# Optimization experiments

Measured on AMD Instinct MI355X. Metric: run time of the kernel, lower is better.

Reference implementation:

```python
import jax, jax.numpy as jnp
import numpy as np

B, P, C = 32, 8732, 21
TOP_K = 200
CONF_THRESH = 0.01
NMS_THRESH = 0.45
VAR0, VAR1 = 0.1, 0.2  # VOC PRIOR_BOX VARIANCE


def setup_inputs() -> dict:
    key = jax.random.key(0)
    k1, k2, k3 = jax.random.split(key, 3)
    loc_data = jax.random.normal(k1, (B, P, 4), jnp.float32)
    conf_data = jax.random.uniform(k2, (B, P, C), jnp.float32)
    prior_data = jax.random.uniform(k3, (P, 4), jnp.float32)
    return {"loc_data": loc_data, "conf_data": conf_data, "prior_data": prior_data}


def _decode(loc, priors):
    # priors are (cx, cy, w, h); returns (x1, y1, x2, y2)
    cxcy = priors[:, :2] + loc[:, :2] * VAR0 * priors[:, 2:]
    wh = priors[:, 2:] * jnp.exp(loc[:, 2:] * VAR1)
    x1y1 = cxcy - wh * 0.5
    return jnp.concatenate([x1y1, x1y1 + wh], axis=1)  # [P,4]


def _nms_class(boxes, scores):
    # boxes [P,4], scores [P] -> [TOP_K,5] rows of (score, x1, y1, x2, y2)
    s = jnp.where(scores > CONF_THRESH, scores, -1.0)
    top_s, idx = jax.lax.top_k(s, TOP_K)          # descending scores
    b = boxes[idx]                                 # [K,4]
    valid = top_s > CONF_THRESH
    x1, y1, x2, y2 = b[:, 0], b[:, 1], b[:, 2], b[:, 3]
    area = (x2 - x1) * (y2 - y1)
    # pairwise intersection / IoU [K,K]
    xx1 = jnp.maximum(x1[:, None], x1[None, :])
    yy1 = jnp.maximum(y1[:, None], y1[None, :])
    xx2 = jnp.minimum(x2[:, None], x2[None, :])
    yy2 = jnp.minimum(y2[:, None], y2[None, :])
    inter = jnp.clip(xx2 - xx1, 0.0) * jnp.clip(yy2 - yy1, 0.0)
    union = area[:, None] + area[None, :] - inter
    iou = inter / union
    ar = jnp.arange(TOP_K)

    def step(carry, j):
        kept, suppressed = carry
        is_kept = valid[j] & ~suppressed[j]
        kept = kept.at[j].set(is_kept)
        suppressed = suppressed | (is_kept & (iou[j] > NMS_THRESH) & (ar > j))
        return (kept, suppressed), None

    (kept, _), _ = jax.lax.scan(
        step, (jnp.zeros(TOP_K, bool), jnp.zeros(TOP_K, bool)), ar)
    # compact kept rows to the front (matches output[i, cl, :count] = ...)
    pos = jnp.cumsum(kept) - 1
    safe = jnp.where(kept, pos, TOP_K)
    rows = jnp.concatenate([top_s[:, None], b], axis=1)  # [K,5]
    out = jnp.zeros((TOP_K + 1, 5), rows.dtype).at[safe].set(rows)[:TOP_K]
    return out


def reference(loc_data, conf_data, prior_data):
    def per_image(loc, conf):
        boxes = _decode(loc, prior_data)           # [P,4]
        return jax.vmap(lambda s: _nms_class(boxes, s), in_axes=1)(conf)  # [C,K,5]

    out = jax.vmap(per_image)(loc_data, conf_data)  # [B,C,K,5]
    return out.at[:, 0].set(0.0)  # class 0 (background) is skipped in original
```

## Files before the change

kernel.cpp:

```cpp
#include <hip/hip_runtime.h>
#include <stdint.h>

#define B_ 32
#define P_ 8732
#define C_ 21
#define TOPK 200
#define TGT 228
#define TGT0 300
#define SUBCAP 28
#define NCH2 35
#define NSLOT (NCH2 * SUBCAP)
#define CONF_T 0.01f
#define NMS_T 0.45f
#define NT 512
#define KV4 5
#define NTASK (B_ * C_)

__device__ __forceinline__ uint32_t f2s(float f) {
    uint32_t u = __float_as_uint(f);
    return (u & 0x80000000u) ? ~u : (u | 0x80000000u);
}
__device__ __forceinline__ float s2f(uint32_t s) {
    uint32_t b = (s & 0x80000000u) ? (s & 0x7FFFFFFFu) : ~s;
    return __uint_as_float(b);
}
__device__ __forceinline__ uint32_t keyof(float v) {
    return f2s((v > CONF_T) ? v : -1.0f);
}
__device__ __forceinline__ uint32_t thr0() {
    return f2s(1.0f - (float)TGT0 / (float)P_);
}

__global__ __launch_bounds__(256) void scatter_cands(const float* __restrict__ conf,
                                                     uint32_t* __restrict__ gccnt,
                                                     uint64_t* __restrict__ gcand) {
    const int b = blockIdx.x / NCH2;
    const int ch = blockIdx.x % NCH2;
    const int p0 = ch * 256;
    const int n = min(256, P_ - p0);
    const int tid = threadIdx.x;
    const int lane = tid & 63;
    const int cs = tid >> 6;
    __shared__ float tile[256 * C_];
    const float4* src4 = (const float4*)(conf + ((size_t)b * P_ + p0) * C_);
    float4* tile4 = (float4*)tile;
    const int tot4 = (n * C_) >> 2;
    for (int i = tid; i < tot4; i += 256) tile4[i] = src4[i];
    __syncthreads();
    const uint32_t T0 = thr0();
    const bool act = (4 * lane) < n;
    for (int c = (cs == 0 ? 4 : cs); c < C_; c += 4) {
        uint32_t kk[4];
        int nq = 0;
        if (act) {
            const float* tp = &tile[4 * lane * C_ + c];
            kk[0] = keyof(tp[0 * C_]);
            kk[1] = keyof(tp[1 * C_]);
            kk[2] = keyof(tp[2 * C_]);
            kk[3] = keyof(tp[3 * C_]);
            nq = (kk[0] >= T0) + (kk[1] >= T0) + (kk[2] >= T0) + (kk[3] >= T0);
        }
        int incl = nq;
        #pragma unroll
        for (int d = 1; d < 64; d <<= 1) {
            int v = __shfl_up(incl, d);
            if (lane >= d) incl += v;
        }
        const int excl = incl - nq;
        const int total = __shfl(incl, 63);
        const int task = b * C_ + c;
        uint64_t* dst = gcand + ((size_t)task * NCH2 + ch) * SUBCAP;
        if (nq) {
            int pos = excl;
            const int pb = p0 + 4 * lane;
            #pragma unroll
            for (int k = 0; k < 4; ++k) {
                if (kk[k] >= T0) {
                    if (pos < SUBCAP)
                        dst[pos] = ((uint64_t)kk[k] << 32) | (uint32_t)(~(uint32_t)(pb + k));
                    ++pos;
                }
            }
        }
        if (lane == 0) gccnt[(size_t)task * NCH2 + ch] = (uint32_t)total;
    }
}

template<bool HASWS>
__global__ __launch_bounds__(NT, 6) void detect_kernel(
    const float* __restrict__ loc, const float* __restrict__ prior,
    const uint32_t* __restrict__ gccnt, const uint64_t* __restrict__ gcand,
    const float* __restrict__ conf, float* __restrict__ out)
{
    const int task = blockIdx.x;
    const int b = task / C_;
    const int c = task % C_;
    const int tid = threadIdx.x;
    const int lane = tid & 63;
    float* outp = out + (size_t)task * TOPK * 5;

    if (c == 0) {
        for (int e = tid; e < TOPK * 5; e += NT) outp[e] = 0.0f;
        return;
    }

    __shared__ uint64_t cand[256];
    __shared__ float4 bbox[TOPK];
    __shared__ float bs[TOPK];
    __shared__ unsigned long long msk[TOPK * 4];
    __shared__ unsigned long long vmask[4];
    __shared__ int order[TOPK];
    __shared__ int s_cnt, s_nk;
    __shared__ int s_c2[2];
    __shared__ uint32_t s_ccnt[NCH2];
    __shared__ int s_gc, s_bad;

    const uint32_t T0 = thr0();

    if (tid == 0) s_cnt = 0;
    if (tid < 2) s_c2[tid] = 0;
    if (HASWS && tid < NCH2) s_ccnt[tid] = gccnt[(size_t)task * NCH2 + tid];
    for (int i2 = tid; i2 < TOPK * 4; i2 += NT) msk[i2] = 0ull;
    __syncthreads();
    if (HASWS && tid < 64) {
        uint32_t cc = (lane < NCH2) ? s_ccnt[lane] : 0u;
        int bad = (cc > SUBCAP) ? 1 : 0;
        int tot = (int)cc;
        #pragma unroll
        for (int d = 1; d < 64; d <<= 1) {
            tot += __shfl_down(tot, d);
            bad |= __shfl_down(bad, d);
        }
        if (lane == 0) { s_gc = tot; s_bad = bad; }
    }
    __syncthreads();

    const bool fast = HASWS && !s_bad && s_gc >= TOPK;
    const int gc = HASWS ? s_gc : 0;

    uint64_t vc0 = 0, vc1 = 0;
    bool val0 = false, val1 = false;
    uint4 kv[KV4];
    if (fast) {
        const uint64_t* gp = gcand + (size_t)task * NSLOT;
        {
            const int ch0 = tid / SUBCAP, i0 = tid - ch0 * SUBCAP;
            if (i0 < (int)s_ccnt[ch0]) { vc0 = gp[tid]; val0 = true; }
        }
        const int s1 = tid + NT;
        if (s1 < NSLOT) {
            const int ch1 = s1 / SUBCAP, i1 = s1 - ch1 * SUBCAP;
            if (i1 < (int)s_ccnt[ch1]) { vc1 = gp[s1]; val1 = true; }
        }
    } else {
        const float* sp = conf + (size_t)b * P_ * C_ + c;
        #pragma unroll
        for (int r = 0; r < KV4; ++r) {
            uint32_t uu[4];
            #pragma unroll
            for (int c4 = 0; c4 < 4; ++c4) {
                int p = (tid + r * NT) * 4 + c4;
                if (p < P_) {
                    float v = sp[(size_t)p * C_];
                    v = (v > CONF_T) ? v : -1.0f;
                    uu[c4] = f2s(v);
                } else uu[c4] = 0u;
            }
            kv[r] = make_uint4(uu[0], uu[1], uu[2], uu[3]);
        }
    }

    if (fast) {
        uint32_t vthr = T0;
        if (gc > 256) {
            const uint32_t k0 = (uint32_t)(vc0 >> 32);
            const uint32_t k1 = (uint32_t)(vc1 >> 32);
            uint32_t lo = T0, hi = 0xFFFFFFFFu;
            uint32_t t;
            {
                const float sc = s2f(T0);
                const float sn = 1.0f - (1.0f - sc) * (float)TGT / (float)gc;
                t = f2s(sn);
                if (!(t > lo && t < hi)) t = lo + ((hi - lo) >> 1);
            }
            for (int it = 0; ; ++it) {
                const int slot = it & 1;
                int my = (val0 && k0 >= t) + (val1 && k1 >= t);
                #pragma unroll
                for (int d = 1; d < 64; d <<= 1) my += __shfl_down(my, d);
                if (lane == 0) atomicAdd(&s_c2[slot], my);
                __syncthreads();
                const int cnt = s_c2[slot];
                __syncthreads();
                if (tid == 0) s_c2[slot] = 0;
                if (cnt >= TOPK && cnt <= 256) { vthr = t; break; }
                if (cnt > 256) lo = t; else hi = t;
                if (hi - lo <= 1) { vthr = lo; break; }
                uint32_t tn = 0;
                bool bis = (it >= 8) || (cnt == 0);
                if (!bis) {
                    const float sc = s2f(t);
                    const float sn = 1.0f - (1.0f - sc) * (float)TGT / (float)cnt;
                    tn = f2s(sn);
                    if (!(tn > lo && tn < hi)) bis = true;
                }
                if (bis) tn = lo + ((hi - lo) >> 1);
                t = tn;
            }
        }
        if (val0 && (uint32_t)(vc0 >> 32) >= vthr) {
            int pos = atomicAdd(&s_cnt, 1);
            if (pos < 256) cand[pos] = vc0;
        }
        if (val1 && (uint32_t)(vc1 >> 32) >= vthr) {
            int pos = atomicAdd(&s_cnt, 1);
            if (pos < 256) cand[pos] = vc1;
        }
    } else {
        uint32_t lo = 0u, hi = 0xFFFFFFFFu;
        uint32_t t = f2s(1.0f - (float)TGT / (float)P_);
        uint32_t vthr = 0u;
        for (int it = 0; ; ++it) {
            const int slot = it & 1;
            int my = 0;
            #pragma unroll
            for (int r = 0; r < KV4; ++r)
                my += (kv[r].x >= t) + (kv[r].y >= t) + (kv[r].z >= t) + (kv[r].w >= t);
            #pragma unroll
            for (int d = 1; d < 64; d <<= 1) my += __shfl_down(my, d);
            if (lane == 0) atomicAdd(&s_c2[slot], my);
            __syncthreads();
            const int cnt = s_c2[slot];
            __syncthreads();
            if (tid == 0) s_c2[slot] = 0;
            if (cnt >= TOPK && cnt <= 256) { vthr = t; break; }
            if (cnt > 256) lo = t; else hi = t;
            if (hi - lo <= 1) { vthr = lo; break; }
            uint32_t tn = 0;
            bool bis = (it >= 8) || (cnt == 0);
            if (!bis) {
                const float sc = s2f(t);
                const float sn = 1.0f - (1.0f - sc) * (float)TGT / (float)cnt;
                tn = f2s(sn);
                if (!(tn > lo && tn < hi)) bis = true;
            }
            if (bis) tn = lo + ((hi - lo) >> 1);
            t = tn;
        }
        #pragma unroll
        for (int r = 0; r < KV4; ++r) {
            const int pb = (tid + r * NT) * 4;
            uint32_t uu[4] = {kv[r].x, kv[r].y, kv[r].z, kv[r].w};
            #pragma unroll
            for (int c4 = 0; c4 < 4; ++c4) {
                uint32_t u = uu[c4];
                if (u >= vthr) {
                    int pos = atomicAdd(&s_cnt, 1);
                    if (pos < 256) cand[pos] = ((uint64_t)u << 32) | (uint32_t)(~(uint32_t)(pb + c4));
                }
            }
        }
    }
    __syncthreads();
    if (tid < 256 && tid >= s_cnt) cand[tid] = 0ull;
    __syncthreads();

    uint64_t v = (tid < 256) ? cand[tid] : 0ull;
    for (int kk = 2; kk <= 256; kk <<= 1) {
        for (int j = kk >> 1; j > 0; j >>= 1) {
            if (j >= 64) {
                __syncthreads();
                if (tid < 256) cand[tid] = v;
                __syncthreads();
                if (tid < 256) {
                    uint64_t pv = cand[tid ^ j];
                    bool keepmax = (((tid & j) == 0) == ((tid & kk) == 0));
                    v = keepmax ? (v > pv ? v : pv) : (v < pv ? v : pv);
                }
            } else if (tid < 256) {
                uint64_t pv = __shfl_xor(v, j);
                bool keepmax = (((tid & j) == 0) == ((tid & kk) == 0));
                v = keepmax ? (v > pv ? v : pv) : (v < pv ? v : pv);
            }
        }
    }

    float my_sc = -1.0f;
    if (tid < TOPK) {
        uint32_t su = (uint32_t)(v >> 32);
        int p = (int)(~(uint32_t)v);
        my_sc = s2f(su);
        const float4 l4 = *(const float4*)(loc + ((size_t)b * P_ + p) * 4);
        const float4 pr = *(const float4*)(prior + (size_t)p * 4);
        float cx = __fadd_rn(pr.x, __fmul_rn(__fmul_rn(l4.x, 0.1f), pr.z));
        float cy = __fadd_rn(pr.y, __fmul_rn(__fmul_rn(l4.y, 0.1f), pr.w));
        float ew = (float)exp((double)__fmul_rn(l4.z, 0.2f));
        float eh = (float)exp((double)__fmul_rn(l4.w, 0.2f));
        float w  = __fmul_rn(pr.z, ew);
        float h  = __fmul_rn(pr.w, eh);
        float x1 = __fsub_rn(cx, __fmul_rn(w, 0.5f));
        float y1 = __fsub_rn(cy, __fmul_rn(h, 0.5f));
        float x2 = __fadd_rn(x1, w);
        float y2 = __fadd_rn(y1, h);
        bs[tid] = my_sc;
        bbox[tid] = make_float4(x1, y1, x2, y2);
    }
    {
        unsigned long long bm = __ballot(tid < TOPK && my_sc > CONF_T);
        if (lane == 0 && tid < 256) vmask[tid >> 6] = bm;
    }
    __syncthreads();

    if (tid < 500) {
        const int rp = tid / 5;
        const int s  = tid - rp * 5;
        #pragma unroll
        for (int pass = 0; pass < 2; ++pass) {
            const int j  = pass ? (199 - rp) : rp;
            const int i0 = j + 1 + s;
            const float4 bj = bbox[j];
            const float  aj = __fmul_rn(__fsub_rn(bj.z, bj.x), __fsub_rn(bj.w, bj.y));
            for (int i = i0; i < TOPK; i += 5) {
                const float4 bi = bbox[i];
                float xx1 = fmaxf(bj.x, bi.x);
                float yy1 = fmaxf(bj.y, bi.y);
                float xx2 = fminf(bj.z, bi.z);
                float yy2 = fminf(bj.w, bi.w);
                float dx = fmaxf(__fsub_rn(xx2, xx1), 0.0f);
                float dy = fmaxf(__fsub_rn(yy2, yy1), 0.0f);
                float inter = __fmul_rn(dx, dy);
                if (inter > 0.0f) {
                    float ai = __fmul_rn(__fsub_rn(bi.z, bi.x), __fsub_rn(bi.w, bi.y));
                    float uni = __fsub_rn(__fadd_rn(aj, ai), inter);
                    float t45 = __fmul_rn(NMS_T, uni);
                    float mar = __fmul_rn(t45, 1e-6f);
                    bool sup;
                    if (inter > __fadd_rn(t45, mar)) sup = true;
                    else if (inter < __fsub_rn(t45, mar)) sup = false;
                    else sup = (inter / uni > NMS_T);
                    if (sup) atomicOr(&msk[j * 4 + (i >> 6)], 1ull << (i & 63));
                }
            }
        }
    }
    __syncthreads();

    if (tid < 64) {
        const int L = tid;
        auto or_reduce = [&](unsigned long long x) {
            #pragma unroll
            for (int d = 1; d < 64; d <<= 1) x |= __shfl_xor(x, d);
            return x;
        };
        unsigned long long s1 = 0, s2 = 0, s3 = 0;
        int nk = 0;
        #pragma unroll
        for (int w = 0; w < 4; ++w) {
            const int j = (w << 6) | L;
            unsigned long long r0 = 0, r1 = 0, r2 = 0, r3 = 0;
            if (j < TOPK) {
                const unsigned long long* mr = &msk[j * 4];
                r0 = mr[0]; r1 = mr[1]; r2 = mr[2]; r3 = mr[3];
            }
            const unsigned long long rself = (w == 0) ? r0 : (w == 1) ? r1
                                           : (w == 2) ? r2 : r3;
            unsigned long long sw = (w == 0) ? 0ull : (w == 1) ? s1
                                  : (w == 2) ? s2 : s3;
            unsigned long long alive = vmask[w] & ~sw;
            unsigned long long pm = 0;
            while (alive) {
                int jl = __ffsll(alive) - 1;
                if (L == 0) order[nk] = (w << 6) | jl;
                ++nk;
                sw |= __shfl(rself, jl);
                pm |= (1ull << jl);
                alive &= ~(sw | (1ull << jl));
            }
            if (pm) {
                const bool picked = (pm >> L) & 1ull;
                if (w == 0) {
                    s1 |= or_reduce(picked ? r1 : 0ull);
                    s2 |= or_reduce(picked ? r2 : 0ull);
                    s3 |= or_reduce(picked ? r3 : 0ull);
                } else if (w == 1) {
                    s2 |= or_reduce(picked ? r2 : 0ull);
                    s3 |= or_reduce(picked ? r3 : 0ull);
                } else if (w == 2) {
                    s3 |= or_reduce(picked ? r3 : 0ull);
                }
            }
        }
        if (L == 0) s_nk = nk;
    }
    __syncthreads();

    const int nk = s_nk;
    for (int e = tid; e < TOPK * 5; e += NT) {
        int r = e / 5;
        int f = e - r * 5;
        float val = 0.0f;
        if (r < nk) {
            int j = order[r];
            float4 bb = bbox[j];
            val = (f == 0) ? bs[j] : (f == 1) ? bb.x : (f == 2) ? bb.y
                : (f == 3) ? bb.z : bb.w;
        }
        outp[e] = val;
    }
}

extern "C" void kernel_launch(void* const* d_in, const int* in_sizes, int n_in,
                              void* d_out, int out_size, void* d_ws, size_t ws_size,
                              hipStream_t stream) {
    const float* loc   = (const float*)d_in[0];
    const float* conf  = (const float*)d_in[1];
    const float* prior = (const float*)d_in[2];
    float* out = (float*)d_out;

    const size_t cnt_bytes  = (size_t)NTASK * NCH2 * sizeof(uint32_t);
    const size_t cand_bytes = (size_t)NTASK * NSLOT * sizeof(uint64_t);
    if (ws_size >= cnt_bytes + cand_bytes) {
        uint32_t* gccnt = (uint32_t*)d_ws;
        uint64_t* gcand = (uint64_t*)((char*)d_ws + cnt_bytes);
        scatter_cands<<<B_ * NCH2, 256, 0, stream>>>(conf, gccnt, gcand);
        detect_kernel<true><<<NTASK, NT, 0, stream>>>(loc, prior, gccnt, gcand, conf, out);
    } else {
        detect_kernel<false><<<NTASK, NT, 0, stream>>>(loc, prior, nullptr, nullptr, conf, out);
    }
}
```

Baseline: 123.0 us.

## Split NMS greedy scan into separate kernel and use ballot-based compaction

Moves the serial single-wavefront greedy NMS scan and output write out of the 512-thread detect kernel into a new 256-thread nms_scan kernel. The suppression masks, boxes and scores go through a workspace buffer, so the large blocks no longer sit idle while one wave runs the scan. It also replaces shuffle prefix sums and per-thread atomics with ballot/popcount compaction and precomputes box areas in shared memory. The cost is an extra launch and a global round trip of about 10KB per task, and the new path only runs when the workspace is large enough.

```diff
diff --git a/kernel.cpp b/kernel.cpp
--- a/kernel.cpp
+++ b/kernel.cpp
@@ -15,6 +15,12 @@
 #define NT 512
 #define KV4 5
 #define NTASK (B_ * C_)
+
+#define TD_STRIDE 10432
+#define TD_MSK   0
+#define TD_VMASK 6400
+#define TD_BBOX  6432
+#define TD_BS    9632
 
 __device__ __forceinline__ uint32_t f2s(float f) {
     uint32_t u = __float_as_uint(f);
@@ -50,28 +56,25 @@
     const uint32_t T0 = thr0();
     const bool act = (4 * lane) < n;
     for (int c = (cs == 0 ? 4 : cs); c < C_; c += 4) {
-        uint32_t kk[4];
-        int nq = 0;
+        uint32_t kk[4] = {0u, 0u, 0u, 0u};
         if (act) {
             const float* tp = &tile[4 * lane * C_ + c];
             kk[0] = keyof(tp[0 * C_]);
             kk[1] = keyof(tp[1 * C_]);
             kk[2] = keyof(tp[2 * C_]);
             kk[3] = keyof(tp[3 * C_]);
-            nq = (kk[0] >= T0) + (kk[1] >= T0) + (kk[2] >= T0) + (kk[3] >= T0);
-        }
-        int incl = nq;
-        #pragma unroll
-        for (int d = 1; d < 64; d <<= 1) {
-            int v = __shfl_up(incl, d);
-            if (lane >= d) incl += v;
-        }
-        const int excl = incl - nq;
-        const int total = __shfl(incl, 63);
+        }
+        const unsigned long long m0 = __ballot(act && kk[0] >= T0);
+        const unsigned long long m1 = __ballot(act && kk[1] >= T0);
+        const unsigned long long m2 = __ballot(act && kk[2] >= T0);
+        const unsigned long long m3 = __ballot(act && kk[3] >= T0);
+        const int total = __popcll(m0) + __popcll(m1) + __popcll(m2) + __popcll(m3);
         const int task = b * C_ + c;
         uint64_t* dst = gcand + ((size_t)task * NCH2 + ch) * SUBCAP;
-        if (nq) {
-            int pos = excl;
+        if (act) {
+            const unsigned long long below = (1ull << lane) - 1ull;
+            int pos = __popcll(m0 & below) + __popcll(m1 & below)
+                    + __popcll(m2 & below) + __popcll(m3 & below);
             const int pb = p0 + 4 * lane;
             #pragma unroll
             for (int k = 0; k < 4; ++k) {
@@ -86,11 +89,12 @@
     }
 }
 
-template<bool HASWS>
+template<bool HASWS, bool SPLIT>
 __global__ __launch_bounds__(NT, 6) void detect_kernel(
     const float* __restrict__ loc, const float* __restrict__ prior,
     const uint32_t* __restrict__ gccnt, const uint64_t* __restrict__ gcand,
-    const float* __restrict__ conf, float* __restrict__ out)
+    const float* __restrict__ conf, float* __restrict__ out,
+    char* __restrict__ tdata)
 {
     const int task = blockIdx.x;
     const int b = task / C_;
@@ -100,17 +104,19 @@
     float* outp = out + (size_t)task * TOPK * 5;
 
     if (c == 0) {
-        for (int e = tid; e < TOPK * 5; e += NT) outp[e] = 0.0f;
+        if constexpr (!SPLIT) {
+            for (int e = tid; e < TOPK * 5; e += NT) outp[e] = 0.0f;
+        }
         return;
     }
 
     __shared__ uint64_t cand[256];
     __shared__ float4 bbox[TOPK];
     __shared__ float bs[TOPK];
+    __shared__ float sar[TOPK];
     __shared__ unsigned long long msk[TOPK * 4];
     __shared__ unsigned long long vmask[4];
-    __shared__ int order[TOPK];
-    __shared__ int s_cnt, s_nk;
+    __shared__ int s_cnt;
     __shared__ int s_c2[2];
     __shared__ uint32_t s_ccnt[NCH2];
     __shared__ int s_gc, s_bad;
@@ -171,10 +177,10 @@
     }
 
     if (fast) {
+        const uint32_t k0 = (uint32_t)(vc0 >> 32);
+        const uint32_t k1 = (uint32_t)(vc1 >> 32);
         uint32_t vthr = T0;
         if (gc > 256) {
-            const uint32_t k0 = (uint32_t)(vc0 >> 32);
-            const uint32_t k1 = (uint32_t)(vc1 >> 32);
             uint32_t lo = T0, hi = 0xFFFFFFFFu;
             uint32_t t;
             {
@@ -208,14 +214,19 @@
                 t = tn;
             }
         }
-        if (val0 && (uint32_t)(vc0 >> 32) >= vthr) {
-            int pos = atomicAdd(&s_cnt, 1);
-            if (pos < 256) cand[pos] = vc0;
-        }
-        if (val1 && (uint32_t)(vc1 >> 32) >= vthr) {
-            int pos = atomicAdd(&s_cnt, 1);
-            if (pos < 256) cand[pos] = vc1;
-        }
+        const bool p0v = val0 && k0 >= vthr;
+        const bool p1v = val1 && k1 >= vthr;
+        const unsigned long long mm0 = __ballot(p0v);
+        const unsigned long long mm1 = __ballot(p1v);
+        const int wtot = __popcll(mm0) + __popcll(mm1);
+        int base = 0;
+        if (lane == 0 && wtot) base = atomicAdd(&s_cnt, wtot);
+        base = __shfl(base, 0);
+        const unsigned long long below = (1ull << lane) - 1ull;
+        const int o0 = base + __popcll(mm0 & below);
+        const int o1 = base + __popcll(mm0) + __popcll(mm1 & below);
+        if (p0v && o0 < 256) cand[o0] = vc0;
+        if (p1v && o1 < 256) cand[o1] = vc1;
     } else {
         uint32_t lo = 0u, hi = 0xFFFFFFFFu;
         uint32_t t = f2s(1.0f - (float)TGT / (float)P_);
@@ -304,6 +315,7 @@
         float y2 = __fadd_rn(y1, h);
         bs[tid] = my_sc;
         bbox[tid] = make_float4(x1, y1, x2, y2);
+        sar[tid] = __fmul_rn(__fsub_rn(x2, x1), __fsub_rn(y2, y1));
     }
     {
         unsigned long long bm = __ballot(tid < TOPK && my_sc > CONF_T);
@@ -319,7 +331,7 @@
             const int j  = pass ? (199 - rp) : rp;
             const int i0 = j + 1 + s;
             const float4 bj = bbox[j];
-            const float  aj = __fmul_rn(__fsub_rn(bj.z, bj.x), __fsub_rn(bj.w, bj.y));
+            const float  aj = sar[j];
             for (int i = i0; i < TOPK; i += 5) {
                 const float4 bi = bbox[i];
                 float xx1 = fmaxf(bj.x, bi.x);
@@ -330,7 +342,7 @@
                 float dy = fmaxf(__fsub_rn(yy2, yy1), 0.0f);
                 float inter = __fmul_rn(dx, dy);
                 if (inter > 0.0f) {
-                    float ai = __fmul_rn(__fsub_rn(bi.z, bi.x), __fsub_rn(bi.w, bi.y));
+                    float ai = sar[i];
                     float uni = __fsub_rn(__fadd_rn(aj, ai), inter);
                     float t45 = __fmul_rn(NMS_T, uni);
                     float mar = __fmul_rn(t45, 1e-6f);
@@ -345,8 +357,123 @@
     }
     __syncthreads();
 
-    if (tid < 64) {
+    if constexpr (SPLIT) {
+        char* td = tdata + (size_t)task * TD_STRIDE;
+        unsigned long long* gm = (unsigned long long*)(td + TD_MSK);
+        for (int i = tid; i < TOPK * 4; i += NT) gm[i] = msk[i];
+        if (tid < 4) ((unsigned long long*)(td + TD_VMASK))[tid] = vmask[tid];
+        if (tid < TOPK) {
+            ((float4*)(td + TD_BBOX))[tid] = bbox[tid];
+            ((float*)(td + TD_BS))[tid] = bs[tid];
+        }
+        return;
+    } else {
+        __shared__ int order[TOPK];
+        __shared__ int s_nk;
+
+        if (tid < 64) {
+            const int L = tid;
+            auto or_reduce = [&](unsigned long long x) {
+                #pragma unroll
+                for (int d = 1; d < 64; d <<= 1) x |= __shfl_xor(x, d);
+                return x;
+            };
+            unsigned long long s1 = 0, s2 = 0, s3 = 0;
+            int nk = 0;
+            #pragma unroll
+            for (int w = 0; w < 4; ++w) {
+                const int j = (w << 6) | L;
+                unsigned long long r0 = 0, r1 = 0, r2 = 0, r3 = 0;
+                if (j < TOPK) {
+                    const unsigned long long* mr = &msk[j * 4];
+                    r0 = mr[0]; r1 = mr[1]; r2 = mr[2]; r3 = mr[3];
+                }
+                const unsigned long long rself = (w == 0) ? r0 : (w == 1) ? r1
+                                               : (w == 2) ? r2 : r3;
+                unsigned long long sw = (w == 0) ? 0ull : (w == 1) ? s1
+                                      : (w == 2) ? s2 : s3;
+                unsigned long long alive = vmask[w] & ~sw;
+                unsigned long long pm = 0;
+                while (alive) {
+                    int jl = __ffsll(alive) - 1;
+                    if (L == 0) order[nk] = (w << 6) | jl;
+                    ++nk;
+                    sw |= __shfl(rself, jl);
+                    pm |= (1ull << jl);
+                    alive &= ~(sw | (1ull << jl));
+                }
+                if (pm) {
+                    const bool picked = (pm >> L) & 1ull;
+                    if (w == 0) {
+                        s1 |= or_reduce(picked ? r1 : 0ull);
+                        s2 |= or_reduce(picked ? r2 : 0ull);
+                        s3 |= or_reduce(picked ? r3 : 0ull);
+                    } else if (w == 1) {
+                        s2 |= or_reduce(picked ? r2 : 0ull);
+                        s3 |= or_reduce(picked ? r3 : 0ull);
+                    } else if (w == 2) {
+                        s3 |= or_reduce(picked ? r3 : 0ull);
+                    }
+                }
+            }
+            if (L == 0) s_nk = nk;
+        }
+        __syncthreads();
+
+        const int nk = s_nk;
+        for (int e = tid; e < TOPK * 5; e += NT) {
+            int r = e / 5;
+            int f = e - r * 5;
+            float val = 0.0f;
+            if (r < nk) {
+                int j = order[r];
+                float4 bb = bbox[j];
+                val = (f == 0) ? bs[j] : (f == 1) ? bb.x : (f == 2) ? bb.y
+                    : (f == 3) ? bb.z : bb.w;
+            }
+            outp[e] = val;
+        }
+    }
+}
+
+__global__ __launch_bounds__(256) void nms_scan(const char* __restrict__ tdata,
+                                                float* __restrict__ out) {
+    const int task = blockIdx.x;
+    const int c = task % C_;
+    const int tid = threadIdx.x;
+    float* outp = out + (size_t)task * TOPK * 5;
+    if (c == 0) {
+        for (int e = tid; e < TOPK * 5; e += 256) outp[e] = 0.0f;
+        return;
+    }
+    const char* td = tdata + (size_t)task * TD_STRIDE;
+    const unsigned long long* gmsk = (const unsigned long long*)(td + TD_MSK);
+    const unsigned long long* gvm  = (const unsigned long long*)(td + TD_VMASK);
+    const float4* gbb = (const float4*)(td + TD_BBOX);
+    const float*  gbs = (const float*)(td + TD_BS);
+
+    __shared__ float4 bbox[TOPK];
+    __shared__ float bs[TOPK];
+    __shared__ int order[TOPK];
+    __shared__ int s_nk;
+
+    if (tid >= 64) {
+        for (int i = tid - 64; i < TOPK; i += 192) { bbox[i] = gbb[i]; bs[i] = gbs[i]; }
+    } else {
         const int L = tid;
+        unsigned long long R[4][4];
+        unsigned long long vm[4];
+        #pragma unroll
+        for (int w = 0; w < 4; ++w) {
+            const int j = (w << 6) | L;
+            unsigned long long r0 = 0, r1 = 0, r2 = 0, r3 = 0;
+            if (j < TOPK) {
+                const unsigned long long* mr = gmsk + (size_t)j * 4;
+                r0 = mr[0]; r1 = mr[1]; r2 = mr[2]; r3 = mr[3];
+            }
+            R[w][0] = r0; R[w][1] = r1; R[w][2] = r2; R[w][3] = r3;
+            vm[w] = gvm[w];
+        }
         auto or_reduce = [&](unsigned long long x) {
             #pragma unroll
             for (int d = 1; d < 64; d <<= 1) x |= __shfl_xor(x, d);
@@ -356,17 +483,10 @@
         int nk = 0;
         #pragma unroll
         for (int w = 0; w < 4; ++w) {
-            const int j = (w << 6) | L;
-            unsigned long long r0 = 0, r1 = 0, r2 = 0, r3 = 0;
-            if (j < TOPK) {
-                const unsigned long long* mr = &msk[j * 4];
-                r0 = mr[0]; r1 = mr[1]; r2 = mr[2]; r3 = mr[3];
-            }
-            const unsigned long long rself = (w == 0) ? r0 : (w == 1) ? r1
-                                           : (w == 2) ? r2 : r3;
+            const unsigned long long rself = R[w][w];
             unsigned long long sw = (w == 0) ? 0ull : (w == 1) ? s1
                                   : (w == 2) ? s2 : s3;
-            unsigned long long alive = vmask[w] & ~sw;
+            unsigned long long alive = vm[w] & ~sw;
             unsigned long long pm = 0;
             while (alive) {
                 int jl = __ffsll(alive) - 1;
@@ -379,14 +499,14 @@
             if (pm) {
                 const bool picked = (pm >> L) & 1ull;
                 if (w == 0) {
-                    s1 |= or_reduce(picked ? r1 : 0ull);
-                    s2 |= or_reduce(picked ? r2 : 0ull);
-                    s3 |= or_reduce(picked ? r3 : 0ull);
+                    s1 |= or_reduce(picked ? R[0][1] : 0ull);
+                    s2 |= or_reduce(picked ? R[0][2] : 0ull);
+                    s3 |= or_reduce(picked ? R[0][3] : 0ull);
                 } else if (w == 1) {
-                    s2 |= or_reduce(picked ? r2 : 0ull);
-                    s3 |= or_reduce(picked ? r3 : 0ull);
+                    s2 |= or_reduce(picked ? R[1][2] : 0ull);
+                    s3 |= or_reduce(picked ? R[1][3] : 0ull);
                 } else if (w == 2) {
-                    s3 |= or_reduce(picked ? r3 : 0ull);
+                    s3 |= or_reduce(picked ? R[2][3] : 0ull);
                 }
             }
         }
@@ -395,7 +515,7 @@
     __syncthreads();
 
     const int nk = s_nk;
-    for (int e = tid; e < TOPK * 5; e += NT) {
+    for (int e = tid; e < TOPK * 5; e += 256) {
         int r = e / 5;
         int f = e - r * 5;
         float val = 0.0f;
@@ -419,12 +539,20 @@
 
     const size_t cnt_bytes  = (size_t)NTASK * NCH2 * sizeof(uint32_t);
     const size_t cand_bytes = (size_t)NTASK * NSLOT * sizeof(uint64_t);
-    if (ws_size >= cnt_bytes + cand_bytes) {
+    const size_t td_bytes   = (size_t)NTASK * TD_STRIDE;
+    if (ws_size >= cnt_bytes + cand_bytes + td_bytes) {
+        uint32_t* gccnt = (uint32_t*)d_ws;
+        uint64_t* gcand = (uint64_t*)((char*)d_ws + cnt_bytes);
+        char* tdata = (char*)d_ws + cnt_bytes + cand_bytes;
+        scatter_cands<<<B_ * NCH2, 256, 0, stream>>>(conf, gccnt, gcand);
+        detect_kernel<true, true><<<NTASK, NT, 0, stream>>>(loc, prior, gccnt, gcand, conf, out, tdata);
+        nms_scan<<<NTASK, 256, 0, stream>>>(tdata, out);
+    } else if (ws_size >= cnt_bytes + cand_bytes) {
         uint32_t* gccnt = (uint32_t*)d_ws;
         uint64_t* gcand = (uint64_t*)((char*)d_ws + cnt_bytes);
         scatter_cands<<<B_ * NCH2, 256, 0, stream>>>(conf, gccnt, gcand);
-        detect_kernel<true><<<NTASK, NT, 0, stream>>>(loc, prior, gccnt, gcand, conf, out);
+        detect_kernel<true, false><<<NTASK, NT, 0, stream>>>(loc, prior, gccnt, gcand, conf, out, nullptr);
     } else {
-        detect_kernel<false><<<NTASK, NT, 0, stream>>>(loc, prior, nullptr, nullptr, conf, out);
-    }
-}
+        detect_kernel<false, false><<<NTASK, NT, 0, stream>>>(loc, prior, nullptr, nullptr, conf, out, nullptr);
+    }
+}
```

Result: no change. 124.7 us (+1.4%).
